# Optimization experiments

Hardware: AMD Instinct MI355X
Metric: run time of the kernel (lower is better)

The kernel has to match this reference:

```python
import jax, jax.numpy as jnp
import numpy as np

B, T, C, K, DILATION = 8, 4096, 1024, 4, 1


def setup_inputs() -> dict:
    key = jax.random.key(0)
    kx, kw = jax.random.split(key)
    x = jax.random.normal(kx, (B, T, C), dtype=jnp.float32)
    # kaiming_uniform_(a=sqrt(5)) on a (C, K) weight: bound = sqrt(6/((1+a^2)*fan_in)) = 1/sqrt(K)
    bound = 1.0 / np.sqrt(K)
    weight = jax.random.uniform(kw, (C, K), dtype=jnp.float32, minval=-bound, maxval=bound)
    return {"x": x, "weight": weight}


def _next_pow2(n: int) -> int:
    return 1 << (int(n) - 1).bit_length()


def reference(x, weight):
    # Faithful FFT-based depthwise causal conv, matching the torch module.
    dilation = DILATION
    C_, Kk = weight.shape
    L_eff = dilation * (Kk - 1) + 1
    left_pad = L_eff - 1

    x_bct = jnp.transpose(x, (0, 2, 1))  # (B, C, T)
    Bb, Cc, Tt = x_bct.shape

    # dilated kernel, then time-reversed (so FFT conv == causal correlation)
    k_eff = jnp.zeros((C_, L_eff), dtype=x.dtype).at[:, ::dilation].set(weight)
    k_rev = jnp.flip(k_eff, axis=-1)

    x_pad = jnp.pad(x_bct, ((0, 0), (0, 0), (left_pad, 0)))  # causal left pad
    target_len = x_pad.shape[-1] + L_eff - 1
    n_fft = _next_pow2(target_len)

    Xf = jnp.fft.rfft(x_pad, n=n_fft)          # (B, C, n_fft//2+1) complex
    Kf = jnp.fft.rfft(k_rev, n=n_fft)          # (C, n_fft//2+1) complex
    y_full = jnp.fft.irfft(Xf * Kf[None], n=n_fft)  # broadcast over batch
    y = y_full[..., left_pad:left_pad + Tt]
    return jnp.transpose(y, (0, 2, 1))  # (B, T, C)
```

## Files before the change

### kernel.cpp

```cpp
#include <hip/hip_runtime.h>


#define T_TILE 16

typedef float f32x4 __attribute__((ext_vector_type(4)));

__device__ __forceinline__ f32x4 load_vec(const float4* p) {
    f32x4 r;
    asm volatile("global_load_dwordx4 %0, %1, off" : "=v"(r) : "v"(p));
    return r;
}

__global__ __launch_bounds__(256, 4) void DepthwiseCausalConv1d_57870389346354_kernel(
    const float4* __restrict__ x,
    const float4* __restrict__ w,
    float4* __restrict__ y,
    int T, int C4)
{
    const int tiles_per_b = T / T_TILE;
    const int tile = blockIdx.x;
    const int b  = tile / tiles_per_b;
    const int t0 = (tile % tiles_per_b) * T_TILE;
    const int c4 = threadIdx.x;

    const float4 w0 = w[4 * c4 + 0];
    const float4 w1 = w[4 * c4 + 1];
    const float4 w2 = w[4 * c4 + 2];
    const float4 w3 = w[4 * c4 + 3];

    const float4* xb = x + (size_t)b * T * C4 + c4;
    float4*       yb = y + (size_t)b * T * C4 + c4;

    f32x4 v[T_TILE + 3];
    v[0] = load_vec(xb + (size_t)((t0 >= 3) ? t0 - 3 : 0) * C4);
    v[1] = load_vec(xb + (size_t)((t0 >= 2) ? t0 - 2 : 0) * C4);
    v[2] = load_vec(xb + (size_t)((t0 >= 1) ? t0 - 1 : 0) * C4);
#pragma unroll
    for (int u = 0; u < T_TILE; ++u)
        v[3 + u] = load_vec(xb + (size_t)(t0 + u) * C4);

    asm volatile("s_waitcnt vmcnt(0)" ::: "memory");
    __builtin_amdgcn_sched_barrier(0);

    if (t0 == 0) {
        v[0] = (f32x4)0.f;
        v[1] = (f32x4)0.f;
        v[2] = (f32x4)0.f;
    }

#pragma unroll
    for (int u = T_TILE - 1; u >= 0; --u) {
        const f32x4 a = v[u], bb = v[u + 1], cc = v[u + 2], dd = v[u + 3];
        f32x4 out;
        out.x = w0.x * a.x + w0.y * bb.x + w0.z * cc.x + w0.w * dd.x;
        out.y = w1.x * a.y + w1.y * bb.y + w1.z * cc.y + w1.w * dd.y;
        out.z = w2.x * a.z + w2.y * bb.z + w2.z * cc.z + w2.w * dd.z;
        out.w = w3.x * a.w + w3.y * bb.w + w3.z * cc.w + w3.w * dd.w;
        v[u + 3] = out;
    }

#pragma unroll
    for (int u = 0; u < T_TILE; ++u)
        __builtin_nontemporal_store(v[3 + u],
                                    (f32x4*)&yb[(size_t)(t0 + u) * C4]);
}

extern "C" void kernel_launch(void* const* d_in, const int* in_sizes, int n_in,
                              void* d_out, int out_size, void* d_ws, size_t ws_size,
                              hipStream_t stream)
{
    (void)in_sizes; (void)n_in; (void)out_size; (void)d_ws; (void)ws_size;
    constexpr int B = 8, T = 4096, C = 1024;

    const float4* x = (const float4*)d_in[0];
    const float4* w = (const float4*)d_in[1];
    float4*       y = (float4*)d_out;

    dim3 block(C / 4);
    dim3 grid(B * (T / T_TILE));

    DepthwiseCausalConv1d_57870389346354_kernel<<<grid, block, 0, stream>>>(
        x, w, y, T, C / 4);
}
```

Before: 47.14 us.

## Double-buffer time tiles per block with staged waits and longer spans

Each block now covers a 32-step time span instead of 16. The span is processed as four 8-row sub-tiles, and the loads for the next sub-tile are issued before the current one is computed. Partial `s_waitcnt` counts let computation and stores overlap with outstanding loads. A sliding three-register window replaces the full register array, and the halo reads per output drop. This halves the grid and removes the explicit occupancy hint. The hand-tuned vmcnt values depend on stores counting in the same counter, which is fragile.

```diff
diff --git a/kernel.cpp b/kernel.cpp
--- a/kernel.cpp
+++ b/kernel.cpp
@@ -1,7 +1,9 @@
 #include <hip/hip_runtime.h>
 
 
-#define T_TILE 16
+#define ROWS 8
+#define TILES 4
+#define T_SPAN (ROWS * TILES)
 
 typedef float f32x4 __attribute__((ext_vector_type(4)));
 
@@ -11,16 +13,15 @@
     return r;
 }
 
-__global__ __launch_bounds__(256, 4) void DepthwiseCausalConv1d_57870389346354_kernel(
+__global__ __launch_bounds__(256) void DepthwiseCausalConv1d_57870389346354_kernel(
     const float4* __restrict__ x,
     const float4* __restrict__ w,
     float4* __restrict__ y,
     int T, int C4)
 {
-    const int tiles_per_b = T / T_TILE;
-    const int tile = blockIdx.x;
-    const int b  = tile / tiles_per_b;
-    const int t0 = (tile % tiles_per_b) * T_TILE;
+    const int spans_per_b = T / T_SPAN;
+    const int b  = blockIdx.x / spans_per_b;
+    const int t0 = (blockIdx.x % spans_per_b) * T_SPAN;
     const int c4 = threadIdx.x;
 
     const float4 w0 = w[4 * c4 + 0];
@@ -31,38 +32,46 @@
     const float4* xb = x + (size_t)b * T * C4 + c4;
     float4*       yb = y + (size_t)b * T * C4 + c4;
 
-    f32x4 v[T_TILE + 3];
-    v[0] = load_vec(xb + (size_t)((t0 >= 3) ? t0 - 3 : 0) * C4);
-    v[1] = load_vec(xb + (size_t)((t0 >= 2) ? t0 - 2 : 0) * C4);
-    v[2] = load_vec(xb + (size_t)((t0 >= 1) ? t0 - 1 : 0) * C4);
+    f32x4 wm3 = load_vec(xb + (size_t)((t0 >= 3) ? t0 - 3 : 0) * C4);
+    f32x4 wm2 = load_vec(xb + (size_t)((t0 >= 2) ? t0 - 2 : 0) * C4);
+    f32x4 wm1 = load_vec(xb + (size_t)((t0 >= 1) ? t0 - 1 : 0) * C4);
+
+    f32x4 tile[2][ROWS];
 #pragma unroll
-    for (int u = 0; u < T_TILE; ++u)
-        v[3 + u] = load_vec(xb + (size_t)(t0 + u) * C4);
-
-    asm volatile("s_waitcnt vmcnt(0)" ::: "memory");
-    __builtin_amdgcn_sched_barrier(0);
-
-    if (t0 == 0) {
-        v[0] = (f32x4)0.f;
-        v[1] = (f32x4)0.f;
-        v[2] = (f32x4)0.f;
-    }
+    for (int u = 0; u < ROWS; ++u)
+        tile[0][u] = load_vec(xb + (size_t)(t0 + u) * C4);
 
 #pragma unroll
-    for (int u = T_TILE - 1; u >= 0; --u) {
-        const f32x4 a = v[u], bb = v[u + 1], cc = v[u + 2], dd = v[u + 3];
-        f32x4 out;
-        out.x = w0.x * a.x + w0.y * bb.x + w0.z * cc.x + w0.w * dd.x;
-        out.y = w1.x * a.y + w1.y * bb.y + w1.z * cc.y + w1.w * dd.y;
-        out.z = w2.x * a.z + w2.y * bb.z + w2.z * cc.z + w2.w * dd.z;
-        out.w = w3.x * a.w + w3.y * bb.w + w3.z * cc.w + w3.w * dd.w;
-        v[u + 3] = out;
-    }
+    for (int k = 0; k < TILES; ++k) {
+        if (k + 1 < TILES) {
+#pragma unroll
+            for (int u = 0; u < ROWS; ++u)
+                tile[(k + 1) & 1][u] =
+                    load_vec(xb + (size_t)(t0 + (k + 1) * ROWS + u) * C4);
+        }
+
+        if (k == 0)              asm volatile("s_waitcnt vmcnt(8)"  ::: "memory");
+        else if (k == TILES - 1) asm volatile("s_waitcnt vmcnt(8)"  ::: "memory");
+        else                     asm volatile("s_waitcnt vmcnt(16)" ::: "memory");
+        __builtin_amdgcn_sched_barrier(0);
+
+        if (k == 0 && t0 == 0) {
+            wm3 = (f32x4)0.f; wm2 = (f32x4)0.f; wm1 = (f32x4)0.f;
+        }
 
 #pragma unroll
-    for (int u = 0; u < T_TILE; ++u)
-        __builtin_nontemporal_store(v[3 + u],
-                                    (f32x4*)&yb[(size_t)(t0 + u) * C4]);
+        for (int u = 0; u < ROWS; ++u) {
+            const f32x4 cur = tile[k & 1][u];
+            f32x4 out;
+            out.x = w0.x * wm3.x + w0.y * wm2.x + w0.z * wm1.x + w0.w * cur.x;
+            out.y = w1.x * wm3.y + w1.y * wm2.y + w1.z * wm1.y + w1.w * cur.y;
+            out.z = w2.x * wm3.z + w2.y * wm2.z + w2.z * wm1.z + w2.w * cur.z;
+            out.w = w3.x * wm3.w + w3.y * wm2.w + w3.z * wm1.w + w3.w * cur.w;
+            __builtin_nontemporal_store(out,
+                (f32x4*)&yb[(size_t)(t0 + k * ROWS + u) * C4]);
+            wm3 = wm2; wm2 = wm1; wm1 = cur;
+        }
+    }
 }
 
 extern "C" void kernel_launch(void* const* d_in, const int* in_sizes, int n_in,
@@ -77,7 +86,7 @@
     float4*       y = (float4*)d_out;
 
     dim3 block(C / 4);
-    dim3 grid(B * (T / T_TILE));
+    dim3 grid(B * (T / T_SPAN));
 
     DepthwiseCausalConv1d_57870389346354_kernel<<<grid, block, 0, stream>>>(
         x, w, y, T, C / 4);
```

Result: faster. 45.89 us (-2.7%).
